# Performance work log

Hardware: AMD Instinct MI355X
Metric: run time of the kernel (lower is better)

## Reference

```python
import jax, jax.numpy as jnp
import numpy as np

N_NODES = 50000
N_EDGES = 800000
N_FEAT = 128
HIDDEN = 256
N_CLASSES = 40
K_HOPS = 10
ALPHA = 0.1


def setup_inputs() -> dict:
    key = jax.random.key(0)
    k1, k2, k3, k4 = jax.random.split(key, 4)
    x = jax.random.normal(k1, (N_NODES, N_FEAT), dtype=jnp.float32)
    edge_index = jax.random.randint(k2, (2, N_EDGES), 0, N_NODES, dtype=jnp.int64)
    # PPR init of gamma weights: temp[k] = alpha*(1-alpha)^k, temp[K] = (1-alpha)^K
    temp_np = ALPHA * (1.0 - ALPHA) ** np.arange(K_HOPS + 1)
    temp_np[-1] = (1.0 - ALPHA) ** K_HOPS
    temp = jnp.asarray(temp_np, dtype=jnp.float32)
    W1 = jax.random.normal(k3, (N_FEAT, HIDDEN), dtype=jnp.float32) * (1.0 / np.sqrt(N_FEAT))
    b1 = jnp.zeros((HIDDEN,), dtype=jnp.float32)
    W2 = jax.random.normal(k4, (HIDDEN, N_CLASSES), dtype=jnp.float32) * (1.0 / np.sqrt(HIDDEN))
    b2 = jnp.zeros((N_CLASSES,), dtype=jnp.float32)
    return {"x": x, "edge_index": edge_index, "temp": temp,
            "W1": W1, "b1": b1, "W2": W2, "b2": b2, "K": K_HOPS}


def reference(x, edge_index, temp, W1, b1, W2, b2, K):
    N = x.shape[0]
    # gcn_norm with self-loops (fill value 1): A_hat = D^-1/2 (A + I) D^-1/2
    loops = jnp.arange(N, dtype=edge_index.dtype)
    row = jnp.concatenate([edge_index[0], loops])  # source (x_j)
    col = jnp.concatenate([edge_index[1], loops])  # target (aggregation)
    ones = jnp.ones(row.shape[0], dtype=x.dtype)
    deg = jax.ops.segment_sum(ones, col, num_segments=N)
    dinv = jnp.where(deg > 0, deg ** -0.5, jnp.zeros_like(deg))
    norm = dinv[row] * dinv[col]  # [E+N]

    # K-hop propagation with learned hop-weighted sum
    h = x
    hidden = temp[0] * x
    for k in range(K):  # small fixed hop count
        msg = norm[:, None] * h[row]                      # gather + scale
        h = jax.ops.segment_sum(msg, col, num_segments=N)  # scatter-add
        hidden = hidden + temp[k + 1] * h

    # eval mode: dropout is a no-op
    z = jax.nn.relu(hidden @ W1 + b1)
    z = z @ W2 + b2
    return jax.nn.log_softmax(z, axis=1)
```

## Files before the change

kernel.cpp:

```cpp
#include <hip/hip_runtime.h>
#include <hip/hip_bf16.h>


#define NFEAT 128
#define HID   256
#define NCLS  40
#define KHOPS 10

typedef __attribute__((ext_vector_type(8))) short short8;
typedef __attribute__((ext_vector_type(4))) float floatx4;

__device__ __forceinline__ float blo(unsigned g) { return __uint_as_float(g << 16); }
__device__ __forceinline__ float bhi(unsigned g) { return __uint_as_float(g & 0xffff0000u); }
__device__ __forceinline__ unsigned f2bf(float x) {
  unsigned u = __float_as_uint(x);
  return (u + 0x7fffu + ((u >> 16) & 1u)) >> 16;
}
__device__ __forceinline__ unsigned bpack(float a, float b) {
  return f2bf(a) | (f2bf(b) << 16);
}

__global__ void k_detect64(const unsigned int* __restrict__ raw, int* __restrict__ flag) {
  __shared__ int any;
  int t = threadIdx.x;
  if (t == 0) any = 0;
  __syncthreads();
  if (raw[2 * t + 1] != 0u) any = 1;
  __syncthreads();
  if (t == 0) flag[0] = (any == 0) ? 1 : 0;
}

__global__ void k_zero(int* __restrict__ p, int n) {
  int i = blockIdx.x * blockDim.x + threadIdx.x;
  if (i < n) p[i] = 0;
}

__global__ void k_count(const int* __restrict__ ei32, const long long* __restrict__ ei64,
                        int E, int N, int* __restrict__ cnt, int* __restrict__ rank,
                        const int* __restrict__ flag) {
  int e = blockIdx.x * blockDim.x + threadIdx.x;
  if (e >= E) return;
  int dst = flag[0] ? (int)ei64[(size_t)E + e] : ei32[(size_t)E + e];
  if ((unsigned)dst < (unsigned)N) rank[e] = atomicAdd(&cnt[dst], 1);
  else rank[e] = -1;
}

__global__ __launch_bounds__(256) void k_scan_a(
    const int* __restrict__ cnt, int* __restrict__ bsum, int n) {
  int t = threadIdx.x;
  int base = blockIdx.x * 1024 + t * 4;
  int s = 0;
  if (base + 3 < n) {
    int4 v = *(const int4*)(cnt + base);
    s = v.x + v.y + v.z + v.w;
  } else {
    #pragma unroll
    for (int j = 0; j < 4; ++j) if (base + j < n) s += cnt[base + j];
  }
  #pragma unroll
  for (int off = 1; off < 64; off <<= 1) s += __shfl_xor(s, off);
  __shared__ int ws[4];
  if ((t & 63) == 0) ws[t >> 6] = s;
  __syncthreads();
  if (t == 0) bsum[blockIdx.x] = ws[0] + ws[1] + ws[2] + ws[3];
}

__global__ void k_scan_mid(int* __restrict__ bsum, int* __restrict__ S,
                           int ntiles, int n) {
  int t = threadIdx.x;
  int lane = t & 63, wid = t >> 6;
  int v = (t < ntiles) ? bsum[t] : 0;
  int x = v;
  #pragma unroll
  for (int off = 1; off < 64; off <<= 1) {
    int u = __shfl_up(x, off);
    if (lane >= off) x += u;
  }
  __shared__ int ws[16];
  if (lane == 63) ws[wid] = x;
  __syncthreads();
  if (wid == 0) {
    int s2 = (lane < 16) ? ws[lane] : 0;
    #pragma unroll
    for (int off = 1; off < 16; off <<= 1) {
      int u = __shfl_up(s2, off);
      if (lane >= off) s2 += u;
    }
    if (lane < 16) ws[lane] = s2;
  }
  __syncthreads();
  int woff = wid ? ws[wid - 1] : 0;
  if (t < ntiles) bsum[t] = x - v + woff;
  if (t == 0) S[n] = ws[15];
}

__global__ __launch_bounds__(256) void k_scan_c(
    const int* __restrict__ cnt, const int* __restrict__ bsum,
    int* __restrict__ S, float* __restrict__ dinv, int n) {
  int t = threadIdx.x;
  int base = blockIdx.x * 1024 + t * 4;
  int v[4];
  if (base + 3 < n) {
    int4 q = *(const int4*)(cnt + base);
    v[0] = q.x; v[1] = q.y; v[2] = q.z; v[3] = q.w;
  } else {
    #pragma unroll
    for (int j = 0; j < 4; ++j) v[j] = (base + j < n) ? cnt[base + j] : 0;
  }
  int tsum = v[0] + v[1] + v[2] + v[3];
  int lane = t & 63, wv = t >> 6;
  int x = tsum;
  #pragma unroll
  for (int off = 1; off < 64; off <<= 1) {
    int u = __shfl_up(x, off);
    if (lane >= off) x += u;
  }
  __shared__ int ws[4];
  if (lane == 63) ws[wv] = x;
  __syncthreads();
  int woff = 0;
  #pragma unroll
  for (int j = 0; j < 4; ++j) if (j < wv) woff += ws[j];
  int run = x - tsum + woff + bsum[blockIdx.x];
  #pragma unroll
  for (int j = 0; j < 4; ++j) {
    int idx = base + j;
    if (idx < n) {
      S[idx] = run;
      dinv[idx] = rsqrtf((float)(v[j] + 1));
      run += v[j];
    }
  }
}

__global__ void k_fill(const int* __restrict__ ei32, const long long* __restrict__ ei64,
                       int E, int N, const int* __restrict__ S,
                       const int* __restrict__ rank, int* __restrict__ csr,
                       const int* __restrict__ flag) {
  int e = blockIdx.x * blockDim.x + threadIdx.x;
  if (e >= E) return;
  int r = rank[e];
  if (r < 0) return;
  int src, dst;
  if (flag[0]) { src = (int)ei64[e]; dst = (int)ei64[(size_t)E + e]; }
  else         { src = ei32[e];      dst = ei32[(size_t)E + e]; }
  if ((unsigned)src >= (unsigned)N) return;
  csr[S[dst] + r] = src;
}

__global__ void k_init(const float* __restrict__ x, const float* __restrict__ dinv,
                       unsigned* __restrict__ p0, int total64) {
  int i = blockIdx.x * blockDim.x + threadIdx.x;
  if (i >= total64) return;
  float2 xv = ((const float2*)x)[i];
  float di = dinv[i >> 6];
  p0[i] = bpack(di * xv.x, di * xv.y);
}

__global__ __launch_bounds__(256) void k_prop(
    const unsigned* __restrict__ pin, unsigned* __restrict__ pout,
    const int* __restrict__ S, const int* __restrict__ csr,
    const float* __restrict__ dinv, int N) {
  int wid = __builtin_amdgcn_readfirstlane(threadIdx.x >> 6);
  int lane = threadIdx.x & 63;
  int node = blockIdx.x * 4 + wid;
  if (node >= N) return;
  int g = lane & 15;
  int e = lane >> 4;
  int s = S[node], en = S[node + 1];
  float acc[8] = {0.f, 0.f, 0.f, 0.f, 0.f, 0.f, 0.f, 0.f};
  for (int p = s; p < en; p += 16) {
    uint4 gd[4];
    float wt[4];
    #pragma unroll
    for (int t = 0; t < 4; ++t) {
      int pj = p + t * 4 + e;
      int sidx = csr[pj < en ? pj : s];
      wt[t] = (pj < en) ? 1.f : 0.f;
      gd[t] = *(const uint4*)(pin + (size_t)sidx * 64 + g * 4);
    }
    #pragma unroll
    for (int t = 0; t < 4; ++t) {
      const unsigned* gu = (const unsigned*)&gd[t];
      #pragma unroll
      for (int u = 0; u < 4; ++u) {
        acc[u * 2]     += wt[t] * blo(gu[u]);
        acc[u * 2 + 1] += wt[t] * bhi(gu[u]);
      }
    }
  }
  #pragma unroll
  for (int u = 0; u < 8; ++u) {
    acc[u] += __shfl_xor(acc[u], 16);
    acc[u] += __shfl_xor(acc[u], 32);
  }
  if (e == 0) {
    float di = dinv[node];
    float dd = di * di;
    uint4 gs = *(const uint4*)(pin + (size_t)node * 64 + g * 4);
    const unsigned* su = (const unsigned*)&gs;
    #pragma unroll
    for (int u = 0; u < 4; ++u) {
      acc[u * 2]     += blo(su[u]);
      acc[u * 2 + 1] += bhi(su[u]);
    }
    uint4 pk;
    pk.x = bpack(dd * acc[0], dd * acc[1]);
    pk.y = bpack(dd * acc[2], dd * acc[3]);
    pk.z = bpack(dd * acc[4], dd * acc[5]);
    pk.w = bpack(dd * acc[6], dd * acc[7]);
    *(uint4*)(pout + (size_t)node * 64 + g * 4) = pk;
  }
}

__global__ void k_combine(const unsigned* __restrict__ pbuf,
                          const float* __restrict__ temp,
                          const float* __restrict__ dinv,
                          unsigned* __restrict__ hid, int N) {
  int i = blockIdx.x * blockDim.x + threadIdx.x;
  int total = N * 64;
  if (i >= total) return;
  size_t slab = (size_t)total;
  float tL = 0.f, tH = 0.f;
  #pragma unroll
  for (int k = 0; k <= KHOPS; ++k) {
    unsigned v = pbuf[slab * k + i];
    float tk = temp[k];
    tL += tk * blo(v);
    tH += tk * bhi(v);
  }
  float inv = 1.f / dinv[i >> 6];
  hid[i] = bpack(tL * inv, tH * inv);
}

__global__ __launch_bounds__(256) void k_gemm1(
    const unsigned short* __restrict__ Ab, const float* __restrict__ W1,
    const float* __restrict__ b1, unsigned short* __restrict__ z1, int M) {
  __shared__ unsigned short As[64][136];
  __shared__ unsigned short Bs[16][128][8];
  int tid = threadIdx.x;
  int m0 = blockIdx.x * 64;
  int n0 = blockIdx.y * 128;
  for (int idx = tid; idx < 64 * 16; idx += 256) {
    int m = idx >> 4, c = idx & 15;
    int row = m0 + m; if (row >= M) row = M - 1;
    uint4 v = *(const uint4*)(Ab + (size_t)row * NFEAT + c * 8);
    *(uint4*)&As[m][c * 8] = v;
  }
  for (int idx = tid; idx < 128 * 128; idx += 256) {
    int k = idx >> 7, n = idx & 127;
    Bs[k >> 3][n][k & 7] = (unsigned short)f2bf(W1[(size_t)k * HID + n0 + n]);
  }
  __syncthreads();
  int lane = tid & 63;
  int q = lane >> 4, r16 = lane & 15;
  int nw = (tid >> 6) * 32;
  floatx4 acc[4][2] = {};
  #pragma unroll
  for (int step = 0; step < 4; ++step) {
    int k0 = step * 32;
    short8 a[4], b[2];
    #pragma unroll
    for (int i = 0; i < 4; ++i)
      a[i] = *(const short8*)&As[i * 16 + r16][k0 + q * 8];
    #pragma unroll
    for (int j = 0; j < 2; ++j)
      b[j] = *(const short8*)&Bs[step * 4 + q][nw + j * 16 + r16][0];
    #pragma unroll
    for (int i = 0; i < 4; ++i)
      #pragma unroll
      for (int j = 0; j < 2; ++j)
        acc[i][j] = __builtin_amdgcn_mfma_f32_16x16x32_bf16(a[i], b[j], acc[i][j], 0, 0, 0);
  }
  __syncthreads();
  unsigned short* Zs = &As[0][0];
  #pragma unroll
  for (int j = 0; j < 2; ++j) {
    int n = nw + j * 16 + r16;
    float bias = b1[n0 + n];
    #pragma unroll
    for (int i = 0; i < 4; ++i) {
      #pragma unroll
      for (int r = 0; r < 4; ++r) {
        int m = i * 16 + q * 4 + r;
        float v = fmaxf(acc[i][j][r] + bias, 0.f);
        Zs[m * 136 + n] = (unsigned short)f2bf(v);
      }
    }
  }
  __syncthreads();
  for (int idx = tid; idx < 64 * 16; idx += 256) {
    int m = idx >> 4, c = idx & 15;
    int row = m0 + m;
    if (row < M) {
      uint4 v = *(const uint4*)&Zs[m * 136 + c * 8];
      *(uint4*)(z1 + (size_t)row * HID + n0 + c * 8) = v;
    }
  }
}

__global__ void k_w2prep(const float* __restrict__ W2, unsigned short* __restrict__ W2t) {
  int i = blockIdx.x * blockDim.x + threadIdx.x;
  if (i >= 48 * 256) return;
  int n = i >> 8, k = i & 255;
  W2t[n * 256 + k] = (n < NCLS) ? (unsigned short)f2bf(W2[(size_t)k * NCLS + n]) : 0;
}

__global__ __launch_bounds__(256) void k_mlp2(
    const unsigned short* __restrict__ z1, const unsigned short* __restrict__ W2t,
    const float* __restrict__ b2, float* __restrict__ out, int N) {
  int tid = threadIdx.x;
  int lane = tid & 63;
  int wv = tid >> 6;
  int node0 = blockIdx.x * 64 + wv * 16;
  int q = lane >> 4, m = lane & 15;
  int arow = node0 + m; if (arow >= N) arow = N - 1;
  const unsigned short* aptr = z1 + (size_t)arow * HID + q * 8;
  const unsigned short* bptr = W2t + (size_t)m * HID + q * 8;
  floatx4 acc[3] = {};
  #pragma unroll
  for (int step = 0; step < 8; ++step) {
    short8 a = *(const short8*)(aptr + step * 32);
    #pragma unroll
    for (int j = 0; j < 3; ++j) {
      short8 b = *(const short8*)(bptr + (size_t)j * 16 * HID + step * 32);
      acc[j] = __builtin_amdgcn_mfma_f32_16x16x32_bf16(a, b, acc[j], 0, 0, 0);
    }
  }
  int c = m;
  bool v2 = (c < NCLS - 32);
  float bb0 = b2[c], bb1 = b2[c + 16];
  float bb2 = v2 ? b2[c + 32] : 0.f;
  #pragma unroll
  for (int r = 0; r < 4; ++r) {
    int node = node0 + q * 4 + r;
    float l0 = acc[0][r] + bb0;
    float l1 = acc[1][r] + bb1;
    float l2 = v2 ? (acc[2][r] + bb2) : -3.4e38f;
    float mx = fmaxf(fmaxf(l0, l1), l2);
    #pragma unroll
    for (int off = 1; off < 16; off <<= 1) mx = fmaxf(mx, __shfl_xor(mx, off));
    float sm = __expf(l0 - mx) + __expf(l1 - mx) + (v2 ? __expf(l2 - mx) : 0.f);
    #pragma unroll
    for (int off = 1; off < 16; off <<= 1) sm += __shfl_xor(sm, off);
    float lse = mx + __logf(sm);
    if (node < N) {
      float* op = out + (size_t)node * NCLS + c;
      op[0] = l0 - lse;
      op[16] = l1 - lse;
      if (v2) op[32] = l2 - lse;
    }
  }
}

extern "C" void kernel_launch(void* const* d_in, const int* in_sizes, int n_in,
                              void* d_out, int out_size, void* d_ws, size_t ws_size,
                              hipStream_t stream) {
  const float*     x    = (const float*)d_in[0];
  const int*       ei32 = (const int*)d_in[1];
  const long long* ei64 = (const long long*)d_in[1];
  const float*     temp = (const float*)d_in[2];
  const float*     W1   = (const float*)d_in[3];
  const float*     b1   = (const float*)d_in[4];
  const float*     W2   = (const float*)d_in[5];
  const float*     b2   = (const float*)d_in[6];
  float* out = (float*)d_out;

  int N = in_sizes[0] / NFEAT;
  int E = in_sizes[1] / 2;

  char* w = (char*)d_ws;
  auto carve = [&](size_t bytes) -> void* {
    void* p = (void*)w;
    w += (bytes + 255) & ~(size_t)255;
    return p;
  };
  int*      flag      = (int*)     carve(4);
  int*      cnt       = (int*)     carve((size_t)N * 4);
  int*      S         = (int*)     carve(((size_t)N + 1) * 4);
  float*    dinv      = (float*)   carve((size_t)N * 4);
  int*      bsum      = (int*)     carve(1024 * 4);
  unsigned short* W2t = (unsigned short*)carve(48 * 256 * 2);
  int*      rank      = (int*)     carve((size_t)E * 4);
  int*      csr       = (int*)     carve((size_t)E * 4);
  unsigned* pbuf      = (unsigned*)carve((size_t)(KHOPS + 1) * N * 64 * 4);
  unsigned* hid       = (unsigned*)carve((size_t)N * 64 * 4);
  unsigned short* z1  = (unsigned short*)carve((size_t)N * HID * 2);

  int ntiles = (N + 1023) / 1024;
  size_t slab = (size_t)N * 64;

  k_detect64<<<1, 256, 0, stream>>>((const unsigned int*)d_in[1], flag);
  k_zero<<<(N + 255) / 256, 256, 0, stream>>>(cnt, N);
  k_count<<<(E + 255) / 256, 256, 0, stream>>>(ei32, ei64, E, N, cnt, rank, flag);
  k_scan_a<<<ntiles, 256, 0, stream>>>(cnt, bsum, N);
  k_scan_mid<<<1, 1024, 0, stream>>>(bsum, S, ntiles, N);
  k_scan_c<<<ntiles, 256, 0, stream>>>(cnt, bsum, S, dinv, N);
  k_fill<<<(E + 255) / 256, 256, 0, stream>>>(ei32, ei64, E, N, S, rank, csr, flag);
  k_init<<<(N * 64 + 255) / 256, 256, 0, stream>>>(x, dinv, pbuf, N * 64);
  k_w2prep<<<48, 256, 0, stream>>>(W2, W2t);

  for (int k = 0; k < KHOPS; ++k) {
    k_prop<<<(N + 3) / 4, 256, 0, stream>>>(
        pbuf + slab * k, pbuf + slab * (k + 1), S, csr, dinv, N);
  }
  k_combine<<<(N * 64 + 255) / 256, 256, 0, stream>>>(pbuf, temp, dinv, hid, N);

  k_gemm1<<<dim3((N + 63) / 64, 2), 256, 0, stream>>>(
      (const unsigned short*)hid, W1, b1, z1, N);
  k_mlp2<<<(N + 63) / 64, 256, 0, stream>>>(z1, W2t, b2, out, N);
}
```

Before: 497.6 us.

## Split propagation features into four column slabs mapped to XCD pairs

Stores each hop buffer as four 32-feature column slabs, so each node row in a slab is 64 bytes. Block IDs are remapped so that each pair of XCDs handles one slab, which makes each XCD's L2 cache only a quarter-width copy of the gathered feature table and should raise L2 hit rates on the random neighbour gathers. Each wavefront now covers 16 edges per step with 4 lanes per row, which needs extra shuffle reductions. csr indices are read with nontemporal loads. init and combine are adjusted for the new layout. The gain depends on the blockIdx-to-XCD round-robin assumption holding.

```diff
diff --git a/kernel.cpp b/kernel.cpp
--- a/kernel.cpp
+++ b/kernel.cpp
@@ -149,38 +149,46 @@
 }
 
 __global__ void k_init(const float* __restrict__ x, const float* __restrict__ dinv,
-                       unsigned* __restrict__ p0, int total64) {
+                       unsigned* __restrict__ p0, int N) {
   int i = blockIdx.x * blockDim.x + threadIdx.x;
-  if (i >= total64) return;
+  if (i >= N * 64) return;
+  int n = i >> 6, c = i & 63;
   float2 xv = ((const float2*)x)[i];
-  float di = dinv[i >> 6];
-  p0[i] = bpack(di * xv.x, di * xv.y);
+  float di = dinv[n];
+  p0[(size_t)(c >> 4) * N * 16 + (size_t)n * 16 + (c & 15)] =
+      bpack(di * xv.x, di * xv.y);
 }
 
 __global__ __launch_bounds__(256) void k_prop(
     const unsigned* __restrict__ pin, unsigned* __restrict__ pout,
     const int* __restrict__ S, const int* __restrict__ csr,
     const float* __restrict__ dinv, int N) {
+  int b = blockIdx.x;
+  int xcd = b & 7;
+  int phase = xcd >> 1;
+  int grp = (b >> 3) * 2 + (xcd & 1);
   int wid = __builtin_amdgcn_readfirstlane(threadIdx.x >> 6);
   int lane = threadIdx.x & 63;
-  int node = blockIdx.x * 4 + wid;
+  int node = grp * 4 + wid;
   if (node >= N) return;
-  int g = lane & 15;
-  int e = lane >> 4;
+  const unsigned* pinp  = pin  + (size_t)phase * N * 16;
+  unsigned*       poutp = pout + (size_t)phase * N * 16;
+  int q = lane & 3;
+  int e = lane >> 2;
   int s = S[node], en = S[node + 1];
   float acc[8] = {0.f, 0.f, 0.f, 0.f, 0.f, 0.f, 0.f, 0.f};
-  for (int p = s; p < en; p += 16) {
-    uint4 gd[4];
-    float wt[4];
-    #pragma unroll
-    for (int t = 0; t < 4; ++t) {
-      int pj = p + t * 4 + e;
-      int sidx = csr[pj < en ? pj : s];
+  for (int p = s; p < en; p += 32) {
+    uint4 gd[2];
+    float wt[2];
+    #pragma unroll
+    for (int t = 0; t < 2; ++t) {
+      int pj = p + t * 16 + e;
+      int sidx = __builtin_nontemporal_load(&csr[pj < en ? pj : s]);
       wt[t] = (pj < en) ? 1.f : 0.f;
-      gd[t] = *(const uint4*)(pin + (size_t)sidx * 64 + g * 4);
-    }
-    #pragma unroll
-    for (int t = 0; t < 4; ++t) {
+      gd[t] = *(const uint4*)(pinp + (size_t)sidx * 16 + q * 4);
+    }
+    #pragma unroll
+    for (int t = 0; t < 2; ++t) {
       const unsigned* gu = (const unsigned*)&gd[t];
       #pragma unroll
       for (int u = 0; u < 4; ++u) {
@@ -191,13 +199,15 @@
   }
   #pragma unroll
   for (int u = 0; u < 8; ++u) {
+    acc[u] += __shfl_xor(acc[u], 4);
+    acc[u] += __shfl_xor(acc[u], 8);
     acc[u] += __shfl_xor(acc[u], 16);
     acc[u] += __shfl_xor(acc[u], 32);
   }
   if (e == 0) {
     float di = dinv[node];
     float dd = di * di;
-    uint4 gs = *(const uint4*)(pin + (size_t)node * 64 + g * 4);
+    uint4 gs = *(const uint4*)(pinp + (size_t)node * 16 + q * 4);
     const unsigned* su = (const unsigned*)&gs;
     #pragma unroll
     for (int u = 0; u < 4; ++u) {
@@ -209,7 +219,7 @@
     pk.y = bpack(dd * acc[2], dd * acc[3]);
     pk.z = bpack(dd * acc[4], dd * acc[5]);
     pk.w = bpack(dd * acc[6], dd * acc[7]);
-    *(uint4*)(pout + (size_t)node * 64 + g * 4) = pk;
+    *(uint4*)(poutp + (size_t)node * 16 + q * 4) = pk;
   }
 }
 
@@ -217,20 +227,23 @@
                           const float* __restrict__ temp,
                           const float* __restrict__ dinv,
                           unsigned* __restrict__ hid, int N) {
-  int i = blockIdx.x * blockDim.x + threadIdx.x;
-  int total = N * 64;
-  if (i >= total) return;
-  size_t slab = (size_t)total;
+  int j = blockIdx.x * blockDim.x + threadIdx.x;
+  int n16 = N * 16;
+  if (j >= n16) return;
+  int p = blockIdx.y;
+  size_t slab = (size_t)N * 64;
+  size_t idx = (size_t)p * n16 + j;
   float tL = 0.f, tH = 0.f;
   #pragma unroll
   for (int k = 0; k <= KHOPS; ++k) {
-    unsigned v = pbuf[slab * k + i];
+    unsigned v = pbuf[slab * k + idx];
     float tk = temp[k];
     tL += tk * blo(v);
     tH += tk * bhi(v);
   }
-  float inv = 1.f / dinv[i >> 6];
-  hid[i] = bpack(tL * inv, tH * inv);
+  int n = j >> 4, w = j & 15;
+  float inv = 1.f / dinv[n];
+  hid[(size_t)n * 64 + p * 16 + w] = bpack(tL * inv, tH * inv);
 }
 
 __global__ __launch_bounds__(256) void k_gemm1(
@@ -397,14 +410,17 @@
   k_scan_mid<<<1, 1024, 0, stream>>>(bsum, S, ntiles, N);
   k_scan_c<<<ntiles, 256, 0, stream>>>(cnt, bsum, S, dinv, N);
   k_fill<<<(E + 255) / 256, 256, 0, stream>>>(ei32, ei64, E, N, S, rank, csr, flag);
-  k_init<<<(N * 64 + 255) / 256, 256, 0, stream>>>(x, dinv, pbuf, N * 64);
+  k_init<<<(N * 64 + 255) / 256, 256, 0, stream>>>(x, dinv, pbuf, N);
   k_w2prep<<<48, 256, 0, stream>>>(W2, W2t);
 
+  int ngrp = (N + 3) / 4;
+  int nblk = ((ngrp + 1) / 2) * 8;
   for (int k = 0; k < KHOPS; ++k) {
-    k_prop<<<(N + 3) / 4, 256, 0, stream>>>(
+    k_prop<<<nblk, 256, 0, stream>>>(
         pbuf + slab * k, pbuf + slab * (k + 1), S, csr, dinv, N);
   }
-  k_combine<<<(N * 64 + 255) / 256, 256, 0, stream>>>(pbuf, temp, dinv, hid, N);
+  k_combine<<<dim3((N * 16 + 255) / 256, 4), 256, 0, stream>>>(
+      pbuf, temp, dinv, hid, N);
 
   k_gemm1<<<dim3((N + 63) / 64, 2), 256, 0, stream>>>(
       (const unsigned short*)hid, W1, b1, z1, N);
```

After: 965.0 us. 93.9% more time.

## Bucket CSR neighbours by source-index quarter to improve gather locality

Applied to the files above, without the earlier changes.

Each destination's neighbour list is split into four buckets by the source node's index range, using a 4N count and offset array. The propagation kernel walks the buckets in order, so at any moment concurrent waves tend to gather from a narrower region of the feature buffer, which is meant to improve L2 hit rates. The inner loop is narrowed from 16 to 8 edges per iteration and the CSR index loads are made nontemporal. In exchange, the scan and count arrays are four times larger, each bucket adds loop overhead and padding waste for low-degree nodes, and an extra kernel computes dinv.

```diff
diff --git a/kernel.cpp b/kernel.cpp
--- a/kernel.cpp
+++ b/kernel.cpp
@@ -35,14 +35,20 @@
   if (i < n) p[i] = 0;
 }
 
-__global__ void k_count(const int* __restrict__ ei32, const long long* __restrict__ ei64,
-                        int E, int N, int* __restrict__ cnt, int* __restrict__ rank,
-                        const int* __restrict__ flag) {
+__global__ void k_count4(const int* __restrict__ ei32, const long long* __restrict__ ei64,
+                         int E, int N, int qdiv, int* __restrict__ cnt4,
+                         int* __restrict__ rank, const int* __restrict__ flag) {
   int e = blockIdx.x * blockDim.x + threadIdx.x;
   if (e >= E) return;
-  int dst = flag[0] ? (int)ei64[(size_t)E + e] : ei32[(size_t)E + e];
-  if ((unsigned)dst < (unsigned)N) rank[e] = atomicAdd(&cnt[dst], 1);
-  else rank[e] = -1;
+  int src, dst;
+  if (flag[0]) { src = (int)ei64[e]; dst = (int)ei64[(size_t)E + e]; }
+  else         { src = ei32[e];      dst = ei32[(size_t)E + e]; }
+  if ((unsigned)dst < (unsigned)N && (unsigned)src < (unsigned)N) {
+    int qtr = src / qdiv;
+    rank[e] = atomicAdd(&cnt4[dst * 4 + qtr], 1);
+  } else {
+    rank[e] = -1;
+  }
 }
 
 __global__ __launch_bounds__(256) void k_scan_a(
@@ -96,7 +102,7 @@
 
 __global__ __launch_bounds__(256) void k_scan_c(
     const int* __restrict__ cnt, const int* __restrict__ bsum,
-    int* __restrict__ S, float* __restrict__ dinv, int n) {
+    int* __restrict__ S, int n) {
   int t = threadIdx.x;
   int base = blockIdx.x * 1024 + t * 4;
   int v[4];
@@ -127,14 +133,20 @@
     int idx = base + j;
     if (idx < n) {
       S[idx] = run;
-      dinv[idx] = rsqrtf((float)(v[j] + 1));
       run += v[j];
     }
   }
 }
 
+__global__ void k_dinv(const int* __restrict__ S4, float* __restrict__ dinv, int N) {
+  int n = blockIdx.x * blockDim.x + threadIdx.x;
+  if (n >= N) return;
+  int d = S4[4 * n + 4] - S4[4 * n];
+  dinv[n] = rsqrtf((float)(d + 1));
+}
+
 __global__ void k_fill(const int* __restrict__ ei32, const long long* __restrict__ ei64,
-                       int E, int N, const int* __restrict__ S,
+                       int E, int N, int qdiv, const int* __restrict__ S4,
                        const int* __restrict__ rank, int* __restrict__ csr,
                        const int* __restrict__ flag) {
   int e = blockIdx.x * blockDim.x + threadIdx.x;
@@ -144,8 +156,8 @@
   int src, dst;
   if (flag[0]) { src = (int)ei64[e]; dst = (int)ei64[(size_t)E + e]; }
   else         { src = ei32[e];      dst = ei32[(size_t)E + e]; }
-  if ((unsigned)src >= (unsigned)N) return;
-  csr[S[dst] + r] = src;
+  int qtr = src / qdiv;
+  csr[S4[dst * 4 + qtr] + r] = src;
 }
 
 __global__ void k_init(const float* __restrict__ x, const float* __restrict__ dinv,
@@ -159,7 +171,7 @@
 
 __global__ __launch_bounds__(256) void k_prop(
     const unsigned* __restrict__ pin, unsigned* __restrict__ pout,
-    const int* __restrict__ S, const int* __restrict__ csr,
+    const int* __restrict__ S4, const int* __restrict__ csr,
     const float* __restrict__ dinv, int N) {
   int wid = __builtin_amdgcn_readfirstlane(threadIdx.x >> 6);
   int lane = threadIdx.x & 63;
@@ -167,25 +179,31 @@
   if (node >= N) return;
   int g = lane & 15;
   int e = lane >> 4;
-  int s = S[node], en = S[node + 1];
+  int4 sA = *(const int4*)(S4 + 4 * node);
+  int s4_4 = S4[4 * node + 4];
+  int qb[5] = { sA.x, sA.y, sA.z, sA.w, s4_4 };
   float acc[8] = {0.f, 0.f, 0.f, 0.f, 0.f, 0.f, 0.f, 0.f};
-  for (int p = s; p < en; p += 16) {
-    uint4 gd[4];
-    float wt[4];
-    #pragma unroll
-    for (int t = 0; t < 4; ++t) {
-      int pj = p + t * 4 + e;
-      int sidx = csr[pj < en ? pj : s];
-      wt[t] = (pj < en) ? 1.f : 0.f;
-      gd[t] = *(const uint4*)(pin + (size_t)sidx * 64 + g * 4);
-    }
-    #pragma unroll
-    for (int t = 0; t < 4; ++t) {
-      const unsigned* gu = (const unsigned*)&gd[t];
+  #pragma unroll
+  for (int qtr = 0; qtr < 4; ++qtr) {
+    int qs = qb[qtr], qe = qb[qtr + 1];
+    for (int p = qs; p < qe; p += 8) {
+      uint4 gd[2];
+      float wt[2];
       #pragma unroll
-      for (int u = 0; u < 4; ++u) {
-        acc[u * 2]     += wt[t] * blo(gu[u]);
-        acc[u * 2 + 1] += wt[t] * bhi(gu[u]);
+      for (int t = 0; t < 2; ++t) {
+        int pj = p + t * 4 + e;
+        int sidx = __builtin_nontemporal_load(&csr[pj < qe ? pj : qs]);
+        wt[t] = (pj < qe) ? 1.f : 0.f;
+        gd[t] = *(const uint4*)(pin + (size_t)sidx * 64 + g * 4);
+      }
+      #pragma unroll
+      for (int t = 0; t < 2; ++t) {
+        const unsigned* gu = (const unsigned*)&gd[t];
+        #pragma unroll
+        for (int u = 0; u < 4; ++u) {
+          acc[u * 2]     += wt[t] * blo(gu[u]);
+          acc[u * 2 + 1] += wt[t] * bhi(gu[u]);
+        }
       }
     }
   }
@@ -368,6 +386,7 @@
 
   int N = in_sizes[0] / NFEAT;
   int E = in_sizes[1] / 2;
+  int qdiv = (N + 3) / 4;
 
   char* w = (char*)d_ws;
   auto carve = [&](size_t bytes) -> void* {
@@ -376,8 +395,8 @@
     return p;
   };
   int*      flag      = (int*)     carve(4);
-  int*      cnt       = (int*)     carve((size_t)N * 4);
-  int*      S         = (int*)     carve(((size_t)N + 1) * 4);
+  int*      cnt4      = (int*)     carve((size_t)N * 4 * 4);
+  int*      S4        = (int*)     carve(((size_t)N * 4 + 1) * 4);
   float*    dinv      = (float*)   carve((size_t)N * 4);
   int*      bsum      = (int*)     carve(1024 * 4);
   unsigned short* W2t = (unsigned short*)carve(48 * 256 * 2);
@@ -387,22 +406,24 @@
   unsigned* hid       = (unsigned*)carve((size_t)N * 64 * 4);
   unsigned short* z1  = (unsigned short*)carve((size_t)N * HID * 2);
 
-  int ntiles = (N + 1023) / 1024;
+  int n4 = N * 4;
+  int ntiles4 = (n4 + 1023) / 1024;
   size_t slab = (size_t)N * 64;
 
   k_detect64<<<1, 256, 0, stream>>>((const unsigned int*)d_in[1], flag);
-  k_zero<<<(N + 255) / 256, 256, 0, stream>>>(cnt, N);
-  k_count<<<(E + 255) / 256, 256, 0, stream>>>(ei32, ei64, E, N, cnt, rank, flag);
-  k_scan_a<<<ntiles, 256, 0, stream>>>(cnt, bsum, N);
-  k_scan_mid<<<1, 1024, 0, stream>>>(bsum, S, ntiles, N);
-  k_scan_c<<<ntiles, 256, 0, stream>>>(cnt, bsum, S, dinv, N);
-  k_fill<<<(E + 255) / 256, 256, 0, stream>>>(ei32, ei64, E, N, S, rank, csr, flag);
+  k_zero<<<(n4 + 255) / 256, 256, 0, stream>>>(cnt4, n4);
+  k_count4<<<(E + 255) / 256, 256, 0, stream>>>(ei32, ei64, E, N, qdiv, cnt4, rank, flag);
+  k_scan_a<<<ntiles4, 256, 0, stream>>>(cnt4, bsum, n4);
+  k_scan_mid<<<1, 1024, 0, stream>>>(bsum, S4, ntiles4, n4);
+  k_scan_c<<<ntiles4, 256, 0, stream>>>(cnt4, bsum, S4, n4);
+  k_dinv<<<(N + 255) / 256, 256, 0, stream>>>(S4, dinv, N);
+  k_fill<<<(E + 255) / 256, 256, 0, stream>>>(ei32, ei64, E, N, qdiv, S4, rank, csr, flag);
   k_init<<<(N * 64 + 255) / 256, 256, 0, stream>>>(x, dinv, pbuf, N * 64);
   k_w2prep<<<48, 256, 0, stream>>>(W2, W2t);
 
   for (int k = 0; k < KHOPS; ++k) {
     k_prop<<<(N + 3) / 4, 256, 0, stream>>>(
-        pbuf + slab * k, pbuf + slab * (k + 1), S, csr, dinv, N);
+        pbuf + slab * k, pbuf + slab * (k + 1), S4, csr, dinv, N);
   }
   k_combine<<<(N * 64 + 255) / 256, 256, 0, stream>>>(pbuf, temp, dinv, hid, N);
 
```

After: 615.2 us. +23.6%, slower.
